# Optimization experiments

Hardware: AMD Instinct MI355X
Metric: run time of the kernel (lower is better)

## Reference

```python
import jax, jax.numpy as jnp
import numpy as np
import math

B, S, D = 2, 2048, 2048
H, KVH, HD = 16, 8, 128  # n_heads, n_kv_heads, head_dim
N_REP = H // KVH
ROPE_THETA = 500000.0
NEG_INF = -1e9


def _rope(t, f):
    # t: (B,S,nh,HD) viewed as pairs; f: (S,HD//2,2) = (cos,sin)
    tp = t.reshape(*t.shape[:-1], HD // 2, 2)          # (B,S,nh,HD//2,2)
    fb = f[:, None]                                     # (S,1,HD//2,2)
    row1 = (tp * fb).sum(-1)                            # x0*c + x1*s
    f_rot = jnp.stack([fb[..., 1], -fb[..., 0]], axis=-1)  # (s, -c)
    row0 = (tp * f_rot).sum(-1)                         # x0*s - x1*c
    return jnp.stack([row0, row1], axis=-1).reshape(t.shape)


def setup_inputs() -> dict:
    key = jax.random.key(0)
    ks = jax.random.split(key, 5)
    x = jax.random.normal(ks[0], (B, S, D), dtype=jnp.float32)
    # RoPE table: (S, HD//2, 2) stacked (cos, sin)
    inv_freq = 1.0 / (ROPE_THETA ** (np.arange(0, HD, 2, dtype=np.float32) / HD))
    t = np.arange(S, dtype=np.float32)
    ang = np.outer(t, inv_freq)                         # (S, HD//2)
    freqs_cis = jnp.asarray(np.stack([np.cos(ang), np.sin(ang)], axis=-1))
    # causal additive mask (S,S)
    mask = jnp.where(jnp.triu(jnp.ones((S, S), dtype=bool), k=1), NEG_INF, 0.0).astype(jnp.float32)
    sc = 1.0 / math.sqrt(D)
    wq = jax.random.normal(ks[1], (D, H * HD), dtype=jnp.float32) * sc
    wk = jax.random.normal(ks[2], (D, KVH * HD), dtype=jnp.float32) * sc
    wv = jax.random.normal(ks[3], (D, KVH * HD), dtype=jnp.float32) * sc
    wo = jax.random.normal(ks[4], (H * HD, D), dtype=jnp.float32) * sc
    return {"x": x, "freqs_cis": freqs_cis, "mask": mask, "wq": wq, "wk": wk, "wv": wv, "wo": wo}


def reference(x, freqs_cis, mask, wq, wk, wv, wo):
    bsz, seqlen, _ = x.shape
    xq = (x @ wq).reshape(bsz, seqlen, H, HD)
    xk = (x @ wk).reshape(bsz, seqlen, KVH, HD)
    xv = (x @ wv).reshape(bsz, seqlen, KVH, HD)
    xq = _rope(xq, freqs_cis)
    xk = _rope(xk, freqs_cis)
    keys = jnp.repeat(xk, N_REP, axis=2)                # (B,S,H,HD)
    values = jnp.repeat(xv, N_REP, axis=2)
    q = xq.transpose(0, 2, 1, 3)                        # (B,H,S,HD)
    k = keys.transpose(0, 2, 1, 3)
    v = values.transpose(0, 2, 1, 3)
    scores = jnp.einsum('bhqd,bhkd->bhqk', q, k) / math.sqrt(HD)
    scores = scores + mask                              # broadcast (S,S)
    probs = jax.nn.softmax(scores.astype(jnp.float32), axis=-1).astype(q.dtype)
    out = jnp.einsum('bhqk,bhkd->bhqd', probs, v)
    out = out.transpose(0, 2, 1, 3).reshape(bsz, seqlen, H * HD)
    return out @ wo
```

## Files before the change

### kernel.cpp

```cpp
#include <hip/hip_runtime.h>

typedef short short8 __attribute__((ext_vector_type(8)));
typedef float v4f __attribute__((ext_vector_type(4)));

#define LOG2E 1.4426950408889634f

__device__ __forceinline__ unsigned short f2bf(float f) {
  unsigned int u = __float_as_uint(f);
  u += 0x7fff + ((u >> 16) & 1);
  return (unsigned short)(u >> 16);
}
__device__ __forceinline__ float b2f(unsigned short h) {
  return __uint_as_float(((unsigned int)h) << 16);
}
__device__ __forceinline__ void gl_lds16(const void* g, void* l) {
  __builtin_amdgcn_global_load_lds((const __attribute__((address_space(1))) void*)g,
                                   (__attribute__((address_space(3))) void*)l, 16, 0, 0);
}

__global__ __launch_bounds__(256) void cvt_f32_bf16(const float* __restrict__ src,
                                                    unsigned short* __restrict__ dst, int n) {
  int i = (blockIdx.x * 256 + threadIdx.x) * 4;
  if (i < n) {
    float4 v = *(const float4*)(src + i);
    ushort4 o;
    o.x = f2bf(v.x); o.y = f2bf(v.y); o.z = f2bf(v.z); o.w = f2bf(v.w);
    *(ushort4*)(dst + i) = o;
  }
}

__global__ __launch_bounds__(256) void transpose_f32_bf16(const float* __restrict__ src,
                                                          unsigned short* __restrict__ dst,
                                                          int srcCols) {
  __shared__ float tile[64][65];
  const int c0 = blockIdx.x * 64;
  const int r0 = blockIdx.y * 64;
  const int t = threadIdx.x;
#pragma unroll
  for (int i = 0; i < 16; ++i) {
    int idx = t + i * 256; int r = idx >> 6, c = idx & 63;
    tile[r][c] = src[(size_t)(r0 + r) * srcCols + c0 + c];
  }
  __syncthreads();
#pragma unroll
  for (int i = 0; i < 16; ++i) {
    int idx = t + i * 256; int r = idx >> 6, c = idx & 63;
    dst[(size_t)(c0 + r) * 2048 + r0 + c] = f2bf(tile[c][r]);
  }
}

template <bool OUT_BF16>
__global__ __launch_bounds__(256) void gemm_bt(const unsigned short* __restrict__ A,
                                               const unsigned short* __restrict__ Bt,
                                               void* __restrict__ Cv,
                                               int M, int N, int K) {
  __shared__ __align__(16) unsigned short As[2][128 * 32];
  __shared__ __align__(16) unsigned short Bs[2][128 * 32];
  const int t = threadIdx.x;
  const int wave = t >> 6, lane = t & 63, quad = lane >> 4, l16 = lane & 15;
  const int tm = blockIdx.y * 128, tn = blockIdx.x * 128;
  const int wm = (wave >> 1) * 64, wn = (wave & 1) * 64;
  v4f acc[4][4];
#pragma unroll
  for (int i = 0; i < 4; ++i)
#pragma unroll
    for (int j = 0; j < 4; ++j) acc[i][j] = (v4f){0.f, 0.f, 0.f, 0.f};

  const int swz = (l16 >> 1) & 3;

  const int s0 = t, s1 = 256 + t;
  const unsigned short* pa0 = A + (size_t)(tm + (s0 >> 2)) * K + ((s0 & 3) ^ ((s0 >> 3) & 3)) * 8;
  const unsigned short* pa1 = A + (size_t)(tm + (s1 >> 2)) * K + ((s1 & 3) ^ ((s1 >> 3) & 3)) * 8;
  const unsigned short* pb0 = Bt + (size_t)(tn + (s0 >> 2)) * K + ((s0 & 3) ^ ((s0 >> 3) & 3)) * 8;
  const unsigned short* pb1 = Bt + (size_t)(tn + (s1 >> 2)) * K + ((s1 & 3) ^ ((s1 >> 3) & 3)) * 8;
  const int dOff0 = (wave * 64) * 8;
  const int dOff1 = (256 + wave * 64) * 8;

  gl_lds16(pa0, &As[0][dOff0]); gl_lds16(pa1, &As[0][dOff1]);
  gl_lds16(pb0, &Bs[0][dOff0]); gl_lds16(pb1, &Bs[0][dOff1]);
  pa0 += 32; pa1 += 32; pb0 += 32; pb1 += 32;

  const int nit = K >> 5;
  for (int it = 0; it < nit; ++it) {
    __syncthreads();
    const int cur = it & 1;
    if (it + 1 < nit) {
      const int nxt = cur ^ 1;
      gl_lds16(pa0, &As[nxt][dOff0]); gl_lds16(pa1, &As[nxt][dOff1]);
      gl_lds16(pb0, &Bs[nxt][dOff0]); gl_lds16(pb1, &Bs[nxt][dOff1]);
      pa0 += 32; pa1 += 32; pb0 += 32; pb1 += 32;
    }
    short8 af[4], bf[4];
#pragma unroll
    for (int mt = 0; mt < 4; ++mt)
      af[mt] = *(const short8*)(&As[cur][(wm + mt * 16 + l16) * 32 + (quad ^ swz) * 8]);
#pragma unroll
    for (int nt = 0; nt < 4; ++nt)
      bf[nt] = *(const short8*)(&Bs[cur][(wn + nt * 16 + l16) * 32 + (quad ^ swz) * 8]);
#pragma unroll
    for (int mt = 0; mt < 4; ++mt)
#pragma unroll
      for (int nt = 0; nt < 4; ++nt)
        acc[mt][nt] = __builtin_amdgcn_mfma_f32_16x16x32_bf16(af[mt], bf[nt], acc[mt][nt], 0, 0, 0);
  }

#pragma unroll
  for (int mt = 0; mt < 4; ++mt)
#pragma unroll
    for (int nt = 0; nt < 4; ++nt)
#pragma unroll
      for (int r = 0; r < 4; ++r) {
        int row = tm + wm + mt * 16 + quad * 4 + r;
        int col = tn + wn + nt * 16 + l16;
        float v = acc[mt][nt][r];
        if (OUT_BF16) ((unsigned short*)Cv)[(size_t)row * N + col] = f2bf(v);
        else          ((float*)Cv)[(size_t)row * N + col] = v;
      }
}

__global__ __launch_bounds__(256) void rope_k(unsigned short* __restrict__ qkv,
                                              const float* __restrict__ freqs) {
  const int bs = blockIdx.x;
  const int s = bs & 2047;
  const float qscale = 0.08838834764831845f;
  unsigned int* row = (unsigned int*)(qkv + (size_t)bs * 4096);
  const float2* fr2 = (const float2*)(freqs + s * 128);
#pragma unroll
  for (int k = 0; k < 6; ++k) {
    int d = threadIdx.x + k * 256;
    float sc = (d < 1024) ? qscale : 1.0f;
    float2 cs = fr2[d & 63];
    unsigned int w = row[d];
    float x0 = b2f((unsigned short)(w & 0xffffu));
    float x1 = b2f((unsigned short)(w >> 16));
    float y0 = (x0 * cs.y - x1 * cs.x) * sc;
    float y1 = (x0 * cs.x + x1 * cs.y) * sc;
    row[d] = ((unsigned int)f2bf(y1) << 16) | (unsigned int)f2bf(y0);
  }
}

__global__ __launch_bounds__(256) void transpose_v(const unsigned short* __restrict__ qkv,
                                                   unsigned short* __restrict__ vt) {
  __shared__ unsigned short tile[64][65];
  const int s0 = blockIdx.x * 64, d0 = blockIdx.y * 64;
  const int bk = blockIdx.z; const int b = bk >> 3, kv = bk & 7;
  const int t = threadIdx.x;
#pragma unroll
  for (int i = 0; i < 16; ++i) {
    int idx = t + i * 256; int r = idx >> 6, c = idx & 63;
    tile[r][c] = qkv[(size_t)(b * 2048 + s0 + r) * 4096 + 3072 + kv * 128 + d0 + c];
  }
  __syncthreads();
#pragma unroll
  for (int i = 0; i < 16; ++i) {
    int idx = t + i * 256; int r = idx >> 6, c = idx & 63;
    vt[((size_t)bk * 128 + d0 + r) * 2048 + s0 + c] = tile[c][r];
  }
}

__global__ __launch_bounds__(256) void attn_k(const unsigned short* __restrict__ qkv,
                                              const unsigned short* __restrict__ vt,
                                              unsigned short* __restrict__ Ob) {
  __shared__ __align__(16) unsigned short Ks[64 * 128];
  __shared__ __align__(16) unsigned short Vs[128 * 64];
  __shared__ __align__(16) unsigned short Ps[4][16 * 64];
  const int t = threadIdx.x, wave = t >> 6, lane = t & 63, quad = lane >> 4, l16 = lane & 15;
  const int jpair = blockIdx.x, h = blockIdx.y, b = blockIdx.z;
  const int kv = h >> 1;

  for (int pass = 0; pass < 2; ++pass) {
    const int qblk = (pass == 0) ? jpair : 31 - jpair;
    const int q0 = qblk * 64;

    short8 qf[4];
    {
      const unsigned short* qp =
          qkv + (size_t)(b * 2048 + q0 + wave * 16 + l16) * 4096 + h * 128 + quad * 8;
#pragma unroll
      for (int kc = 0; kc < 4; ++kc) qf[kc] = *(const short8*)(qp + kc * 32);
    }
    v4f oa[8];
#pragma unroll
    for (int i = 0; i < 8; ++i) oa[i] = (v4f){0.f, 0.f, 0.f, 0.f};
    float m_s = -3.0e38f, l_s = 0.f;

    for (int jt = 0; jt <= qblk; ++jt) {
      __syncthreads();
#pragma unroll
      for (int issue = 0; issue < 4; ++issue) {
        int s = issue * 256 + t;
        gl_lds16(qkv + (size_t)(b * 2048 + jt * 64 + (s >> 4)) * 4096 + 2048 + kv * 128 +
                     (((s & 15) ^ ((s >> 4) & 15)) * 8),
                 Ks + (issue * 256 + wave * 64) * 8);
        gl_lds16(vt + ((size_t)(b * 8 + kv) * 128 + (s >> 3)) * 2048 + jt * 64 +
                     (((s & 7) ^ ((s >> 3) & 7)) * 8),
                 Vs + (issue * 256 + wave * 64) * 8);
      }
      __syncthreads();

      v4f st[4];
#pragma unroll
      for (int mt = 0; mt < 4; ++mt) st[mt] = (v4f){0.f, 0.f, 0.f, 0.f};
#pragma unroll
      for (int kc = 0; kc < 4; ++kc)
#pragma unroll
        for (int mt = 0; mt < 4; ++mt) {
          short8 kf = *(const short8*)(Ks + (mt * 16 + l16) * 128 + (((kc * 4 + quad) ^ l16) * 8));
          st[mt] = __builtin_amdgcn_mfma_f32_16x16x32_bf16(kf, qf[kc], st[mt], 0, 0, 0);
        }

      const bool diag = (jt == qblk);
      float mx = -3.0e38f;
#pragma unroll
      for (int mt = 0; mt < 4; ++mt)
#pragma unroll
        for (int r = 0; r < 4; ++r) {
          float v = st[mt][r];
          if (diag && (mt * 16 + quad * 4 + r > wave * 16 + l16)) v = -1.0e30f;
          st[mt][r] = v;
          mx = fmaxf(mx, v);
        }
      mx = fmaxf(mx, __shfl_xor(mx, 16));
      mx = fmaxf(mx, __shfl_xor(mx, 32));
      float mn = fmaxf(m_s, mx);
      float alpha = exp2f((m_s - mn) * LOG2E);
      m_s = mn;
      float lt = 0.f;
#pragma unroll
      for (int mt = 0; mt < 4; ++mt)
#pragma unroll
        for (int r = 0; r < 4; ++r) {
          float p = exp2f((st[mt][r] - mn) * LOG2E);
          st[mt][r] = p;
          lt += p;
        }
      lt += __shfl_xor(lt, 16);
      lt += __shfl_xor(lt, 32);
      l_s = l_s * alpha + lt;

      float a_q[4];
#pragma unroll
      for (int r = 0; r < 4; ++r) a_q[r] = __shfl(alpha, quad * 4 + r);
#pragma unroll
      for (int nt = 0; nt < 8; ++nt)
#pragma unroll
        for (int r = 0; r < 4; ++r) oa[nt][r] *= a_q[r];

#pragma unroll
      for (int mt = 0; mt < 4; ++mt) {
        int pcp = ((mt * 2 + (quad >> 1)) ^ (l16 & 7));
        ushort4 w;
        w.x = f2bf(st[mt][0]); w.y = f2bf(st[mt][1]);
        w.z = f2bf(st[mt][2]); w.w = f2bf(st[mt][3]);
        *(ushort4*)(&Ps[wave][l16 * 64 + pcp * 8 + (quad & 1) * 4]) = w;
      }
      asm volatile("s_waitcnt lgkmcnt(0)" ::: "memory");

      short8 pf[2];
#pragma unroll
      for (int kc2 = 0; kc2 < 2; ++kc2)
        pf[kc2] = *(const short8*)(&Ps[wave][l16 * 64 + (((kc2 * 4 + quad) ^ (l16 & 7)) * 8)]);
#pragma unroll
      for (int nt = 0; nt < 8; ++nt)
#pragma unroll
        for (int kc2 = 0; kc2 < 2; ++kc2) {
          short8 vf = *(const short8*)(Vs + (nt * 16 + l16) * 64 +
                                       (((kc2 * 4 + quad) ^ (l16 & 7)) * 8));
          oa[nt] = __builtin_amdgcn_mfma_f32_16x16x32_bf16(pf[kc2], vf, oa[nt], 0, 0, 0);
        }
    }

    float inv[4];
#pragma unroll
    for (int r = 0; r < 4; ++r) inv[r] = 1.0f / __shfl(l_s, quad * 4 + r);
#pragma unroll
    for (int r = 0; r < 4; ++r) {
      int row = b * 2048 + q0 + wave * 16 + quad * 4 + r;
#pragma unroll
      for (int nt = 0; nt < 8; ++nt)
        Ob[(size_t)row * 2048 + h * 128 + nt * 16 + l16] = f2bf(oa[nt][r] * inv[r]);
    }
    __syncthreads();
  }
}

extern "C" void kernel_launch(void* const* d_in, const int* in_sizes, int n_in,
                              void* d_out, int out_size, void* d_ws, size_t ws_size,
                              hipStream_t stream) {
  (void)in_sizes; (void)n_in; (void)out_size; (void)ws_size;
  const float* x  = (const float*)d_in[0];
  const float* fr = (const float*)d_in[1];
  const float* wq = (const float*)d_in[3];
  const float* wk = (const float*)d_in[4];
  const float* wv = (const float*)d_in[5];
  const float* wo = (const float*)d_in[6];
  float* out = (float*)d_out;

  char* ws = (char*)d_ws;
  unsigned short* Xb    = (unsigned short*)(ws);
  unsigned short* WqkvT = (unsigned short*)(ws + (size_t)(16u << 20));
  unsigned short* WoT   = (unsigned short*)(ws + (size_t)(32u << 20));
  unsigned short* QKV   = (unsigned short*)(ws + (size_t)(40u << 20));
  unsigned short* Vt    = (unsigned short*)(ws);
  unsigned short* Ob    = (unsigned short*)(ws + (size_t)(16u << 20));

  cvt_f32_bf16<<<8192, 256, 0, stream>>>(x, Xb, 2 * 2048 * 2048);
  transpose_f32_bf16<<<dim3(32, 32), 256, 0, stream>>>(wq, WqkvT, 2048);
  transpose_f32_bf16<<<dim3(16, 32), 256, 0, stream>>>(wk, WqkvT + (size_t)2048 * 2048, 1024);
  transpose_f32_bf16<<<dim3(16, 32), 256, 0, stream>>>(wv, WqkvT + (size_t)3072 * 2048, 1024);
  transpose_f32_bf16<<<dim3(32, 32), 256, 0, stream>>>(wo, WoT, 2048);
  gemm_bt<true><<<dim3(32, 32), 256, 0, stream>>>(Xb, WqkvT, QKV, 4096, 4096, 2048);
  rope_k<<<4096, 256, 0, stream>>>(QKV, fr);
  transpose_v<<<dim3(32, 2, 16), 256, 0, stream>>>(QKV, Vt);
  attn_k<<<dim3(16, 16, 2), 256, 0, stream>>>(QKV, Vt, Ob);
  gemm_bt<false><<<dim3(16, 32), 256, 0, stream>>>(Ob, WoT, out, 4096, 2048, 2048);
}
```

Measured before the change: 381.4 us.

## Use 256x256-tile 8-wave pipelined GEMM for fused QKV projection

Adds a new bf16 GEMM kernel with 256x256 output tiles, 512 threads (8 waves), double-buffered LDS filled by direct global-to-LDS loads with an XOR swizzle. The k-loop is split into four MFMA phases interleaved with staged prefetches, with s_setprio raising priority around the MFMA blocks, and block IDs are remapped for L2 locality. It is used only for the QKV projection and aims to cut global and LDS traffic per FLOP while overlapping loads with compute. In exchange the larger tile yields only 256 workgroups, which may underfill the GPU, and the heavy barrier use adds synchronization cost.

```diff
diff --git a/kernel.cpp b/kernel.cpp
--- a/kernel.cpp
+++ b/kernel.cpp
@@ -118,6 +118,163 @@
       }
 }
 
+template <bool OUT_BF16>
+__global__ __launch_bounds__(512, 2) void gemm256(const unsigned short* __restrict__ A,
+                                                  const unsigned short* __restrict__ Bt,
+                                                  void* __restrict__ Cv,
+                                                  int M, int N, int K) {
+  __shared__ __align__(16) unsigned short As[2][256 * 64];
+  __shared__ __align__(16) unsigned short Bs[2][256 * 64];
+  const int t = threadIdx.x;
+  const int wave = t >> 6, lane = t & 63, quad = lane >> 4, l16 = lane & 15;
+  const int wr = wave >> 2, wc = wave & 3;
+
+  const int gx = N >> 8;
+  int id = blockIdx.y * gridDim.x + blockIdx.x;
+  const int nwg = gridDim.x * gridDim.y;
+  id = (id & 7) * (nwg >> 3) + (id >> 3);
+  const int tm = (id / gx) << 8, tn = (id % gx) << 8;
+
+  v4f acc[8][4];
+#pragma unroll
+  for (int i = 0; i < 8; ++i)
+#pragma unroll
+    for (int j = 0; j < 4; ++j) acc[i][j] = (v4f){0.f, 0.f, 0.f, 0.f};
+
+  const int s0 = t, s1 = 512 + t;
+  const size_t hA = (size_t)128 * K;
+  const unsigned short* a0 = A + (size_t)(tm + (s0 >> 3)) * K + ((s0 & 7) ^ ((s0 >> 3) & 7)) * 8;
+  const unsigned short* a1 = A + (size_t)(tm + (s1 >> 3)) * K + ((s1 & 7) ^ ((s1 >> 3) & 7)) * 8;
+  const unsigned short* b0 = Bt + (size_t)(tn + (s0 >> 3)) * K + ((s0 & 7) ^ ((s0 >> 3) & 7)) * 8;
+  const unsigned short* b1 = Bt + (size_t)(tn + (s1 >> 3)) * K + ((s1 & 7) ^ ((s1 >> 3) & 7)) * 8;
+  const int d0 = (wave * 64) * 8;
+  const int d1 = (512 + wave * 64) * 8;
+
+#define STG_A(buf, h, koff)                                         \
+  do {                                                              \
+    gl_lds16(a0 + (size_t)(h) * hA + (koff), &As[buf][(h) * 8192 + d0]); \
+    gl_lds16(a1 + (size_t)(h) * hA + (koff), &As[buf][(h) * 8192 + d1]); \
+  } while (0)
+#define STG_B(buf, h, koff)                                         \
+  do {                                                              \
+    gl_lds16(b0 + (size_t)(h) * hA + (koff), &Bs[buf][(h) * 8192 + d0]); \
+    gl_lds16(b1 + (size_t)(h) * hA + (koff), &Bs[buf][(h) * 8192 + d1]); \
+  } while (0)
+
+  const int aBase = (wr * 128 + l16) * 64;
+  const int bBase = (wc * 64 + l16) * 64;
+  const int c0 = (quad ^ (l16 & 7)) * 8;
+  const int c1 = ((4 + quad) ^ (l16 & 7)) * 8;
+
+  const int nkt = K >> 6;
+
+  STG_A(0, 0, 0); STG_A(0, 1, 0);
+  STG_B(0, 0, 0); STG_B(0, 1, 0);
+  STG_B(1, 0, 64); STG_A(1, 0, 64);
+  asm volatile("s_waitcnt vmcnt(4)" ::: "memory");
+  __builtin_amdgcn_s_barrier();
+
+  short8 af[4][2], bf[4][2];
+  for (int kt = 0; kt < nkt; ++kt) {
+    const int cur = kt & 1, nxt = cur ^ 1;
+    const int koff = kt << 6;
+
+#pragma unroll
+    for (int m = 0; m < 4; ++m) {
+      af[m][0] = *(const short8*)(&As[cur][aBase + m * 1024 + c0]);
+      af[m][1] = *(const short8*)(&As[cur][aBase + m * 1024 + c1]);
+    }
+#pragma unroll
+    for (int n = 0; n < 2; ++n) {
+      bf[n][0] = *(const short8*)(&Bs[cur][bBase + n * 1024 + c0]);
+      bf[n][1] = *(const short8*)(&Bs[cur][bBase + n * 1024 + c1]);
+    }
+    if (kt + 1 < nkt) { STG_A(nxt, 1, koff + 64); STG_B(nxt, 1, koff + 64); }
+    __builtin_amdgcn_s_barrier();
+    asm volatile("s_waitcnt lgkmcnt(0)" ::: "memory");
+    __builtin_amdgcn_s_setprio(1);
+#pragma unroll
+    for (int m = 0; m < 4; ++m)
+#pragma unroll
+      for (int n = 0; n < 2; ++n) {
+        acc[m][n] = __builtin_amdgcn_mfma_f32_16x16x32_bf16(af[m][0], bf[n][0], acc[m][n], 0, 0, 0);
+        acc[m][n] = __builtin_amdgcn_mfma_f32_16x16x32_bf16(af[m][1], bf[n][1], acc[m][n], 0, 0, 0);
+      }
+    __builtin_amdgcn_s_setprio(0);
+    __builtin_amdgcn_s_barrier();
+
+#pragma unroll
+    for (int n = 2; n < 4; ++n) {
+      bf[n][0] = *(const short8*)(&Bs[cur][bBase + n * 1024 + c0]);
+      bf[n][1] = *(const short8*)(&Bs[cur][bBase + n * 1024 + c1]);
+    }
+    __builtin_amdgcn_s_barrier();
+    asm volatile("s_waitcnt lgkmcnt(0)" ::: "memory");
+    __builtin_amdgcn_s_setprio(1);
+#pragma unroll
+    for (int m = 0; m < 4; ++m)
+#pragma unroll
+      for (int n = 2; n < 4; ++n) {
+        acc[m][n] = __builtin_amdgcn_mfma_f32_16x16x32_bf16(af[m][0], bf[n][0], acc[m][n], 0, 0, 0);
+        acc[m][n] = __builtin_amdgcn_mfma_f32_16x16x32_bf16(af[m][1], bf[n][1], acc[m][n], 0, 0, 0);
+      }
+    __builtin_amdgcn_s_setprio(0);
+    __builtin_amdgcn_s_barrier();
+
+#pragma unroll
+    for (int m = 0; m < 4; ++m) {
+      af[m][0] = *(const short8*)(&As[cur][aBase + (4 + m) * 1024 + c0]);
+      af[m][1] = *(const short8*)(&As[cur][aBase + (4 + m) * 1024 + c1]);
+    }
+    if (kt + 2 < nkt) STG_B(cur, 0, koff + 128);
+    __builtin_amdgcn_s_barrier();
+    asm volatile("s_waitcnt lgkmcnt(0)" ::: "memory");
+    __builtin_amdgcn_s_setprio(1);
+#pragma unroll
+    for (int m = 0; m < 4; ++m)
+#pragma unroll
+      for (int n = 0; n < 2; ++n) {
+        acc[4 + m][n] = __builtin_amdgcn_mfma_f32_16x16x32_bf16(af[m][0], bf[n][0], acc[4 + m][n], 0, 0, 0);
+        acc[4 + m][n] = __builtin_amdgcn_mfma_f32_16x16x32_bf16(af[m][1], bf[n][1], acc[4 + m][n], 0, 0, 0);
+      }
+    __builtin_amdgcn_s_setprio(0);
+    __builtin_amdgcn_s_barrier();
+
+    if (kt + 2 < nkt) {
+      STG_A(cur, 0, koff + 128);
+      asm volatile("s_waitcnt vmcnt(4)" ::: "memory");
+    } else {
+      asm volatile("s_waitcnt vmcnt(0)" ::: "memory");
+    }
+    __builtin_amdgcn_s_barrier();
+    __builtin_amdgcn_s_setprio(1);
+#pragma unroll
+    for (int m = 0; m < 4; ++m)
+#pragma unroll
+      for (int n = 2; n < 4; ++n) {
+        acc[4 + m][n] = __builtin_amdgcn_mfma_f32_16x16x32_bf16(af[m][0], bf[n][0], acc[4 + m][n], 0, 0, 0);
+        acc[4 + m][n] = __builtin_amdgcn_mfma_f32_16x16x32_bf16(af[m][1], bf[n][1], acc[4 + m][n], 0, 0, 0);
+      }
+    __builtin_amdgcn_s_setprio(0);
+    __builtin_amdgcn_s_barrier();
+  }
+#undef STG_A
+#undef STG_B
+
+#pragma unroll
+  for (int mf = 0; mf < 8; ++mf)
+#pragma unroll
+    for (int nf = 0; nf < 4; ++nf)
+#pragma unroll
+      for (int r = 0; r < 4; ++r) {
+        int row = tm + wr * 128 + mf * 16 + quad * 4 + r;
+        int col = tn + wc * 64 + nf * 16 + l16;
+        float v = acc[mf][nf][r];
+        if (OUT_BF16) ((unsigned short*)Cv)[(size_t)row * N + col] = f2bf(v);
+        else          ((float*)Cv)[(size_t)row * N + col] = v;
+      }
+}
+
 __global__ __launch_bounds__(256) void rope_k(unsigned short* __restrict__ qkv,
                                               const float* __restrict__ freqs) {
   const int bs = blockIdx.x;
@@ -309,7 +466,7 @@
   transpose_f32_bf16<<<dim3(16, 32), 256, 0, stream>>>(wk, WqkvT + (size_t)2048 * 2048, 1024);
   transpose_f32_bf16<<<dim3(16, 32), 256, 0, stream>>>(wv, WqkvT + (size_t)3072 * 2048, 1024);
   transpose_f32_bf16<<<dim3(32, 32), 256, 0, stream>>>(wo, WoT, 2048);
-  gemm_bt<true><<<dim3(32, 32), 256, 0, stream>>>(Xb, WqkvT, QKV, 4096, 4096, 2048);
+  gemm256<true><<<dim3(16, 16), 512, 0, stream>>>(Xb, WqkvT, QKV, 4096, 4096, 2048);
   rope_k<<<4096, 256, 0, stream>>>(QKV, fr);
   transpose_v<<<dim3(32, 2, 16), 256, 0, stream>>>(QKV, Vt);
   attn_k<<<dim3(16, 16, 2), 256, 0, stream>>>(QKV, Vt, Ob);
```

After: 364.0 us. 4.6% less time.
